# Kernel optimization log

Measured on AMD Instinct MI355X. Metric: run time of the kernel, lower is better.

The kernel has to match this reference:

```python
import jax, jax.numpy as jnp
import numpy as np

NUM_CLASSES = 81
IOU_THR = 0.5
NEG_POS_RATIO = 3


def _cxcywh_to_xyxy(b):
    cx, cy, w, h = b[..., 0], b[..., 1], b[..., 2], b[..., 3]
    return jnp.stack([cx - w / 2, cy - h / 2, cx + w / 2, cy + h / 2], axis=-1)


def _xyxy_to_cxcywh(b):
    x1, y1, x2, y2 = b[..., 0], b[..., 1], b[..., 2], b[..., 3]
    return jnp.stack([(x1 + x2) / 2, (y1 + y2) / 2, x2 - x1, y2 - y1], axis=-1)


def _iou(b1, b2):
    # b1 (M,4), b2 (A,4) in xyxy -> (M,A) pairwise IoU
    lt = jnp.maximum(b1[:, None, :2], b2[None, :, :2])
    rb = jnp.minimum(b1[:, None, 2:], b2[None, :, 2:])
    wh = jnp.clip(rb - lt, 0.0)
    inter = wh[..., 0] * wh[..., 1]
    a1 = (b1[:, 2] - b1[:, 0]) * (b1[:, 3] - b1[:, 1])
    a2 = (b2[:, 2] - b2[:, 0]) * (b2[:, 3] - b2[:, 1])
    union = a1[:, None] + a2[None, :] - inter
    return inter / (union + 1e-7)


def _match_one(gt_boxes, gt_labels, anchors_xyxy, anchors_cxcywh):
    # gt_boxes (M,4) xyxy, gt_labels (M,) -> per-anchor targets
    M = gt_boxes.shape[0]
    iou = _iou(gt_boxes, anchors_xyxy)          # (M, A)
    gt_best_iou = iou.max(axis=1)               # best anchor per GT
    gt_best_idx = iou.argmax(axis=1)
    a_best_iou = iou.max(axis=0)                # best GT per anchor
    a_best_idx = iou.argmax(axis=0)
    pos = a_best_iou > IOU_THR

    # sequential force-assignment (faithful to the torch per-object loop)
    def body(j, carry):
        pos, a_idx = carry
        ba = gt_best_idx[j]
        valid = gt_best_iou[j] > 1e-5
        pos = pos.at[ba].set(jnp.where(valid, True, pos[ba]))
        override = valid & (a_best_iou[ba] < gt_best_iou[j])
        a_idx = a_idx.at[ba].set(jnp.where(override, j, a_idx[ba]))
        return pos, a_idx

    pos, a_idx = jax.lax.fori_loop(0, M, body, (pos, a_best_idx))
    mb = _xyxy_to_cxcywh(gt_boxes[a_idx])       # (A,4) matched GT in cxcywh
    acx = anchors_cxcywh
    enc = jnp.stack([
        (mb[:, 0] - acx[:, 0]) / acx[:, 2],
        (mb[:, 1] - acx[:, 1]) / acx[:, 3],
        jnp.log(mb[:, 2] / acx[:, 2] + 1e-7),
        jnp.log(mb[:, 3] / acx[:, 3] + 1e-7)], axis=-1)
    true_locs = jnp.where(pos[:, None], enc, 0.0)
    true_cls = jnp.where(pos, gt_labels[a_idx] + 1, 0)
    return true_locs, true_cls, pos


def setup_inputs() -> dict:
    key = jax.random.key(0)
    kb, kl, kcx, kwh, kax, kaw, ks = jax.random.split(key, 7)
    B, A, M, C = 32, 24564, 20, NUM_CLASSES
    cxy = 0.2 + 0.6 * jax.random.uniform(kcx, (B, M, 2))
    wh = 0.05 + 0.25 * jax.random.uniform(kwh, (B, M, 2))
    gt_boxes = jnp.concatenate([cxy - wh / 2, cxy + wh / 2], axis=-1)  # valid xyxy
    gt_labels = jax.random.randint(kl, (B, M), 0, C - 1)
    acxy = jax.random.uniform(kax, (A, 2))
    awh = 0.04 + 0.3 * jax.random.uniform(kaw, (A, 2))
    anchors_cxcywh = jnp.concatenate([acxy, awh], axis=-1)
    predicted_locs = jax.random.normal(kb, (B, A, 4), jnp.float32)
    predicted_scores = jax.random.normal(ks, (B, A, C), jnp.float32)
    return {"predicted_locs": predicted_locs, "predicted_scores": predicted_scores,
            "gt_boxes": gt_boxes, "gt_labels": gt_labels,
            "anchors_cxcywh": anchors_cxcywh}


def reference(predicted_locs, predicted_scores, gt_boxes, gt_labels, anchors_cxcywh):
    B, A, C = predicted_scores.shape
    anchors_xyxy = _cxcywh_to_xyxy(anchors_cxcywh)
    true_locs, true_cls, pos = jax.vmap(_match_one, in_axes=(0, 0, None, None))(
        gt_boxes, gt_labels, anchors_xyxy, anchors_cxcywh)
    # SmoothL1 (beta=1, reduction='sum') over positive anchors only
    d = jnp.abs(predicted_locs - true_locs)
    sl1 = jnp.where(d < 1.0, 0.5 * d * d, d - 0.5)
    loc_loss = jnp.sum(sl1 * pos[..., None])
    # per-anchor cross entropy
    logp = jax.nn.log_softmax(predicted_scores, axis=-1)
    conf_all = -jnp.take_along_axis(logp, true_cls[..., None], axis=-1)[..., 0]  # (B,A)
    # hard negative mining
    n_pos = pos.sum(axis=1)                                   # (B,)
    n_keep = jnp.where(n_pos > 0,
                       jnp.minimum(NEG_POS_RATIO * n_pos, A - n_pos),
                       jnp.minimum(NEG_POS_RATIO * 20, A))
    neg_scores = jnp.where(pos, -jnp.inf, conf_all)           # positives never selected
    order = jnp.argsort(-neg_scores, axis=1)                  # descending
    ranks = jnp.argsort(order, axis=1)                        # 0 == hardest negative
    hard_neg = (ranks < n_keep[:, None]) & ~pos
    final_mask = pos | hard_neg
    conf_loss = jnp.sum(conf_all * final_mask)
    n_pos_total = jnp.maximum(n_pos.sum(), 1).astype(jnp.float32)
    total = (loc_loss + conf_loss) / n_pos_total
    return total, loc_loss / n_pos_total, conf_loss / n_pos_total
```

## Files before the change

### kernel.cpp

```cpp
#include <hip/hip_runtime.h>
#include <float.h>
#include <stdint.h>

#define NEG_POS_RATIO 3
#define MAXM 64
#define CHUNK 1024

__device__ __forceinline__ float smooth_l1(float d) {
    float a = fabsf(d);
    return a < 1.0f ? 0.5f * a * a : a - 0.5f;
}
__device__ __forceinline__ unsigned key_of(float f) {
    unsigned u = __float_as_uint(f);
    return (u & 0x80000000u) ? ~u : (u | 0x80000000u);
}
__device__ __forceinline__ float val_of(unsigned k) {
    return __uint_as_float((k & 0x80000000u) ? (k ^ 0x80000000u) : ~k);
}

__global__ void __launch_bounds__(256) k_init(
    unsigned long long* __restrict__ gbest, float* __restrict__ loc_loss,
    float* __restrict__ pos_conf, int* __restrict__ n_pos, int BM, int B)
{
    const int t = blockIdx.x * blockDim.x + threadIdx.x;
    if (t < BM) gbest[t] = 0ULL;
    if (t < B) { loc_loss[t] = 0.0f; pos_conf[t] = 0.0f; n_pos[t] = 0; }
}

__global__ void __launch_bounds__(256) k_gtbest(
    const float*  __restrict__ gt_boxes,
    const float4* __restrict__ anchors,
    int A, int M,
    unsigned long long* __restrict__ gbest)
{
    const int b = blockIdx.y, tid = threadIdx.x;
    const int base = blockIdx.x * CHUNK;
    __shared__ float              s_gt[MAXM * 4];
    __shared__ unsigned long long s_best[MAXM];
    if (tid < M * 4) s_gt[tid] = gt_boxes[(size_t)b * M * 4 + tid];
    if (tid < M) s_best[tid] = 0ULL;
    __syncthreads();

    float ax1[4], ay1[4], ax2[4], ay2[4], aarea[4];
    bool  val[4];
#pragma unroll
    for (int i = 0; i < 4; ++i) {
        const int a = base + tid + i * 256;
        val[i] = a < A;
        if (val[i]) {
            const float4 an = anchors[a];
            const float hx = an.z * 0.5f, hy = an.w * 0.5f;
            ax1[i] = an.x - hx; ay1[i] = an.y - hy;
            ax2[i] = an.x + hx; ay2[i] = an.y + hy;
            aarea[i] = an.z * an.w;
        } else { ax1[i]=ay1[i]=ax2[i]=ay2[i]=aarea[i]=0.0f; }
    }
    for (int j = 0; j < M; ++j) {
        const float gx1 = s_gt[4*j+0], gy1 = s_gt[4*j+1];
        const float gx2 = s_gt[4*j+2], gy2 = s_gt[4*j+3];
        const float garea = (gx2 - gx1) * (gy2 - gy1);
        unsigned long long best = 0ULL;
#pragma unroll
        for (int i = 0; i < 4; ++i) {
            if (!val[i]) continue;
            const float w = fmaxf(fminf(gx2, ax2[i]) - fmaxf(gx1, ax1[i]), 0.0f);
            const float h = fmaxf(fminf(gy2, ay2[i]) - fmaxf(gy1, ay1[i]), 0.0f);
            const float inter = w * h;
            const float iou = inter / ((garea + aarea[i] - inter) + 1e-7f);
            const unsigned a_idx = (unsigned)(base + tid + i * 256);
            const unsigned long long pk =
                ((unsigned long long)__float_as_uint(iou) << 32)
              | (unsigned long long)(0xFFFFFFFFu - a_idx);
            if (pk > best) best = pk;
        }
#pragma unroll
        for (int off = 32; off; off >>= 1) {
            const unsigned long long o = __shfl_xor(best, off);
            if (o > best) best = o;
        }
        if ((tid & 63) == 0) atomicMax(&s_best[j], best);
    }
    __syncthreads();
    if (tid < M) atomicMax(&gbest[(size_t)b * M + tid], s_best[tid]);
}

__global__ void __launch_bounds__(256) k_assign(
    const float4* __restrict__ pred_locs,
    const float*  __restrict__ gt_boxes,
    const int*    __restrict__ gt_labels,
    const float4* __restrict__ anchors,
    int A, int M,
    const unsigned long long* __restrict__ gbest,
    float* __restrict__ loc_loss, int* __restrict__ n_pos,
    int* __restrict__ cls_out)
{
    const int b = blockIdx.y, tid = threadIdx.x;
    const int base = blockIdx.x * CHUNK;
    __shared__ float s_gt[MAXM * 4];
    __shared__ int   s_lab[MAXM];
    __shared__ float s_gbi[MAXM];
    __shared__ int   s_gbx[MAXM];
    if (tid < M * 4) s_gt[tid] = gt_boxes[(size_t)b * M * 4 + tid];
    if (tid < M) {
        s_lab[tid] = gt_labels[(size_t)b * M + tid];
        const unsigned long long v = gbest[(size_t)b * M + tid];
        s_gbi[tid] = __uint_as_float((unsigned)(v >> 32));
        s_gbx[tid] = (int)(0xFFFFFFFFu - (unsigned)(v & 0xFFFFFFFFull));
    }
    __syncthreads();

    float lsum = 0.0f;
    int   np   = 0;
#pragma unroll
    for (int i = 0; i < 4; ++i) {
        const int a = base + tid + i * 256;
        if (a >= A) continue;
        const float4 an = anchors[a];
        const float hx = an.z * 0.5f, hy = an.w * 0.5f;
        const float ax1 = an.x - hx, ay1 = an.y - hy;
        const float ax2 = an.x + hx, ay2 = an.y + hy;
        const float aarea = an.z * an.w;
        float abest = -1.0f; int aidx = 0;
        for (int j = 0; j < M; ++j) {
            const float gx1 = s_gt[4*j+0], gy1 = s_gt[4*j+1];
            const float gx2 = s_gt[4*j+2], gy2 = s_gt[4*j+3];
            const float garea = (gx2 - gx1) * (gy2 - gy1);
            const float w = fmaxf(fminf(gx2, ax2) - fmaxf(gx1, ax1), 0.0f);
            const float h = fmaxf(fminf(gy2, ay2) - fmaxf(gy1, ay1), 0.0f);
            const float inter = w * h;
            const float iou = inter / ((garea + aarea - inter) + 1e-7f);
            if (iou > abest) { abest = iou; aidx = j; }
        }
        bool pos = abest > 0.5f;
        int midx = aidx;
        for (int j = 0; j < M; ++j) {
            if (s_gbx[j] == a && s_gbi[j] > 1e-5f) {
                pos = true;
                if (abest < s_gbi[j]) midx = j;
            }
        }
        int cls = 0;
        if (pos) {
            const float gx1 = s_gt[4*midx+0], gy1 = s_gt[4*midx+1];
            const float gx2 = s_gt[4*midx+2], gy2 = s_gt[4*midx+3];
            const float mcx = (gx1 + gx2) * 0.5f, mcy = (gy1 + gy2) * 0.5f;
            const float mw = gx2 - gx1, mh = gy2 - gy1;
            const float e0 = (mcx - an.x) / an.z;
            const float e1 = (mcy - an.y) / an.w;
            const float e2 = logf(mw / an.z + 1e-7f);
            const float e3 = logf(mh / an.w + 1e-7f);
            const float4 p = pred_locs[(size_t)b * A + a];
            lsum += smooth_l1(p.x - e0) + smooth_l1(p.y - e1)
                  + smooth_l1(p.z - e2) + smooth_l1(p.w - e3);
            ++np;
            cls = s_lab[midx] + 1;
        }
        cls_out[(size_t)b * A + a] = cls;
    }
#pragma unroll
    for (int off = 32; off; off >>= 1) {
        lsum += __shfl_xor(lsum, off);
        np   += __shfl_xor(np, off);
    }
    if ((tid & 63) == 0) {
        atomicAdd(&loc_loss[b], lsum);
        atomicAdd(&n_pos[b], np);
    }
}

__global__ void __launch_bounds__(256) k_conf(
    const float* __restrict__ scores,
    const int*   __restrict__ cls_arr,
    float* __restrict__ pos_conf,
    unsigned* __restrict__ keys,
    int A, int C, int total)
{
    const int tid  = threadIdx.x;
    const int wav  = tid >> 6;
    const int lane = tid & 63;
    const int g    = lane >> 4;
    const int sub  = lane & 15;
    const int row  = (blockIdx.x * 4 + wav) * 4 + g;

    float s  = 0.0f;
    float sc = -FLT_MAX;
    int   cls = 0;
    const bool active = row < total;
    if (active) {
        cls = cls_arr[row];
        const float* rp = scores + (size_t)row * C;
        for (int idx = sub; idx < C; idx += 16) {
            const float v = rp[idx];
            s += __expf(v);
            if (idx == cls) sc = v;
        }
    }
#pragma unroll
    for (int off = 8; off; off >>= 1) {
        s  += __shfl_xor(s, off);
        sc  = fmaxf(sc, __shfl_xor(sc, off));
    }
    if (active && sub == 0) {
        const float conf = __logf(s) - sc;
        if (cls > 0) {
            atomicAdd(&pos_conf[row / A], conf);
            keys[row] = 0u;
        } else {
            keys[row] = key_of(conf);
        }
    }
}

__global__ void __launch_bounds__(256) k_select(
    const unsigned* __restrict__ keys, const int* __restrict__ n_pos,
    float* __restrict__ neg_conf, int A, int M)
{
    const int b   = blockIdx.x;
    const int tid = threadIdx.x;
    const int lane = tid & 63;
    const unsigned* kb = keys + (size_t)b * A;
    const int np = n_pos[b];
    const int k = (np > 0) ? min(NEG_POS_RATIO * np, A - np)
                           : min(NEG_POS_RATIO * M, A);
    __shared__ int      hist[256];
    __shared__ unsigned s_pref;
    __shared__ int      s_rem;
    if (k <= 0) { if (tid == 0) neg_conf[b] = 0.0f; return; }
    if (tid == 0) { s_pref = 0u; s_rem = k; }
    __syncthreads();

    for (int pass = 0; pass < 4; ++pass) {
        const int shift = 24 - 8 * pass;
        hist[tid] = 0;
        __syncthreads();
        const unsigned pref = s_pref;
        for (int a = tid; a < A; a += blockDim.x) {
            const unsigned key = kb[a];
            const bool ok = (pass == 0) || ((key >> (shift + 8)) == (pref >> (shift + 8)));
            if (ok) {
                const int bin = (key >> shift) & 255;
                unsigned long long mm = __ballot(1);
#pragma unroll
                for (int bit = 0; bit < 8; ++bit) {
                    const unsigned long long bb = __ballot((bin >> bit) & 1);
                    mm &= ((bin >> bit) & 1) ? bb : ~bb;
                }
                if ((mm & ((1ULL << lane) - 1)) == 0)
                    atomicAdd(&hist[bin], (int)__popcll(mm));
            }
        }
        __syncthreads();
        if (tid == 0) {
            int rem = s_rem, cum = 0, bsel = 0;
            for (int i = 255; i >= 0; --i) {
                const int c = hist[i];
                if (cum + c >= rem) { bsel = i; s_rem = rem - cum; break; }
                cum += c;
            }
            s_pref = pref | ((unsigned)bsel << shift);
        }
        __syncthreads();
    }
    const unsigned kth = s_pref;
    float sum = 0.0f; int cnt = 0;
    for (int a = tid; a < A; a += blockDim.x) {
        const unsigned key = kb[a];
        if (key > kth) { sum += val_of(key); ++cnt; }
    }
#pragma unroll
    for (int off = 32; off; off >>= 1) {
        sum += __shfl_xor(sum, off);
        cnt += __shfl_xor(cnt, off);
    }
    __shared__ float s_sum[4];
    __shared__ int   s_cnt[4];
    const int w = tid >> 6;
    if (lane == 0) { s_sum[w] = sum; s_cnt[w] = cnt; }
    __syncthreads();
    if (tid == 0) {
        float ts = 0.0f; int tc = 0;
        for (int i = 0; i < (int)(blockDim.x >> 6); ++i) { ts += s_sum[i]; tc += s_cnt[i]; }
        neg_conf[b] = ts + (float)(k - tc) * val_of(kth);
    }
}

__global__ void __launch_bounds__(64) k_final(
    const float* __restrict__ loc_loss,
    const float* __restrict__ pos_conf,
    const float* __restrict__ neg_conf,
    const int*   __restrict__ n_pos,
    int B, float* __restrict__ out)
{
    const int tid = threadIdx.x;
    float L = 0.0f, Cs = 0.0f;
    int   np = 0;
    for (int b = tid; b < B; b += 64) {
        L  += loc_loss[b];
        Cs += pos_conf[b] + neg_conf[b];
        np += n_pos[b];
    }
#pragma unroll
    for (int off = 32; off; off >>= 1) {
        L  += __shfl_xor(L, off);
        Cs += __shfl_xor(Cs, off);
        np += __shfl_xor(np, off);
    }
    if (tid == 0) {
        const float denom = (float)(np > 1 ? np : 1);
        out[0] = (L + Cs) / denom;
        out[1] = L / denom;
        out[2] = Cs / denom;
    }
}

extern "C" void kernel_launch(void* const* d_in, const int* in_sizes, int n_in,
                              void* d_out, int out_size, void* d_ws, size_t ws_size,
                              hipStream_t stream) {
    const float* pred_locs = (const float*)d_in[0];
    const float* scores    = (const float*)d_in[1];
    const float* gt_boxes  = (const float*)d_in[2];
    const int*   gt_labels = (const int*)d_in[3];
    const float* anchors   = (const float*)d_in[4];

    const int A = in_sizes[4] / 4;
    const int B = (int)((long long)in_sizes[0] / (4LL * A));
    const int M = in_sizes[3] / B;
    const int C = (int)((long long)in_sizes[1] / ((long long)B * A));
    float* out = (float*)d_out;

    char* ws = (char*)d_ws;
    float* loc_loss = (float*)ws;
    float* pos_conf = loc_loss + B;
    float* neg_conf = pos_conf + B;
    int*   n_pos    = (int*)(neg_conf + B);
    size_t off = (size_t)(((16LL * B) + 255) / 256) * 256;
    unsigned long long* gbest = (unsigned long long*)(ws + off);
    off += (size_t)(((8LL * B * M) + 255) / 256) * 256;
    int*      cls_arr = (int*)(ws + off);
    unsigned* keys    = (unsigned*)(ws + off + (size_t)B * A * sizeof(int));

    const int NCHUNK = (A + CHUNK - 1) / CHUNK;

    k_init<<<(B * M + 255) / 256, 256, 0, stream>>>(gbest, loc_loss, pos_conf, n_pos,
                                                    B * M, B);
    k_gtbest<<<dim3(NCHUNK, B), 256, 0, stream>>>(gt_boxes, (const float4*)anchors,
                                                  A, M, gbest);
    k_assign<<<dim3(NCHUNK, B), 256, 0, stream>>>((const float4*)pred_locs, gt_boxes,
                                                  gt_labels, (const float4*)anchors,
                                                  A, M, gbest, loc_loss, n_pos, cls_arr);

    const int total = (int)((long long)B * A);
    const int nblk = (total + 15) / 16;
    k_conf<<<dim3((unsigned)nblk), 256, 0, stream>>>(scores, cls_arr, pos_conf, keys,
                                                     A, C, total);

    k_select<<<B, 256, 0, stream>>>(keys, n_pos, neg_conf, A, M);

    k_final<<<1, 64, 0, stream>>>(loc_loss, pos_conf, neg_conf, n_pos, B, out);
}
```

Measured before the change: 803.9 us.

## Stage score rows through LDS with float4 loads and widen select to 1024 threads

k_conf now loads 128 rows of scores per block cooperatively into shared memory with float4 loads, then has two threads per row compute log-sum-exp and gather the target logit. This replaces strided 16-lane row reads. k_select moves to 1024-thread blocks and reads keys as uint4 in the radix-select histogram and final sum passes. The LDS tile hardcodes 81 columns and assumes 16-byte alignment of each block's start. The larger LDS footprint may reduce occupancy.

```diff
diff --git a/kernel.cpp b/kernel.cpp
--- a/kernel.cpp
+++ b/kernel.cpp
@@ -5,6 +5,7 @@
 #define NEG_POS_RATIO 3
 #define MAXM 64
 #define CHUNK 1024
+#define ROWS_PER_BLK 128
 
 __device__ __forceinline__ float smooth_l1(float d) {
     float a = fabsf(d);
@@ -176,30 +177,42 @@
     int A, int C, int total)
 {
     const int tid  = threadIdx.x;
-    const int wav  = tid >> 6;
-    const int lane = tid & 63;
-    const int g    = lane >> 4;
-    const int sub  = lane & 15;
-    const int row  = (blockIdx.x * 4 + wav) * 4 + g;
-
+    const int row0 = blockIdx.x * ROWS_PER_BLK;
+    __shared__ float lds[ROWS_PER_BLK * 81];
+
+    const float* gp = scores + (size_t)row0 * C;
+    const int nrows = min(ROWS_PER_BLK, total - row0);
+    const int nf = nrows * C;
+    const int nv = nf >> 2;
+    const float4* gp4 = (const float4*)gp;
+    float4* l4 = (float4*)lds;
+    for (int i = tid; i < nv; i += 256) l4[i] = gp4[i];
+    for (int i = (nv << 2) + tid; i < nf; i += 256) lds[i] = gp[i];
+    __syncthreads();
+
+    const int rloc = tid >> 1;
+    const int sub  = tid & 1;
+    const int row  = row0 + rloc;
+    const bool active = rloc < nrows;
     float s  = 0.0f;
     float sc = -FLT_MAX;
     int   cls = 0;
-    const bool active = row < total;
     if (active) {
         cls = cls_arr[row];
-        const float* rp = scores + (size_t)row * C;
-        for (int idx = sub; idx < C; idx += 16) {
-            const float v = rp[idx];
-            s += __expf(v);
-            if (idx == cls) sc = v;
-        }
-    }
-#pragma unroll
-    for (int off = 8; off; off >>= 1) {
-        s  += __shfl_xor(s, off);
-        sc  = fmaxf(sc, __shfl_xor(sc, off));
-    }
+        const float* rp = lds + rloc * 81;
+        const int base = sub * 41;
+#pragma unroll 8
+        for (int i = 0; i < 41; ++i) {
+            const int idx = base + i;
+            if (idx < 81) {
+                const float v = rp[idx];
+                s += __expf(v);
+                if (idx == cls) sc = v;
+            }
+        }
+    }
+    s  += __shfl_xor(s, 1);
+    sc  = fmaxf(sc, __shfl_xor(sc, 1));
     if (active && sub == 0) {
         const float conf = __logf(s) - sc;
         if (cls > 0) {
@@ -211,12 +224,29 @@
     }
 }
 
-__global__ void __launch_bounds__(256) k_select(
+__device__ __forceinline__ void hist_add(
+    int* hist, unsigned key, unsigned pref, int shift, bool first, int lane)
+{
+    const bool ok = first || ((key >> (shift + 8)) == (pref >> (shift + 8)));
+    if (ok) {
+        const int bin = (key >> shift) & 255;
+        unsigned long long mm = __ballot(1);
+#pragma unroll
+        for (int bit = 0; bit < 8; ++bit) {
+            const unsigned long long bb = __ballot((bin >> bit) & 1);
+            mm &= ((bin >> bit) & 1) ? bb : ~bb;
+        }
+        if ((mm & ((1ULL << lane) - 1)) == 0)
+            atomicAdd(&hist[bin], (int)__popcll(mm));
+    }
+}
+
+__global__ void __launch_bounds__(1024) k_select(
     const unsigned* __restrict__ keys, const int* __restrict__ n_pos,
     float* __restrict__ neg_conf, int A, int M)
 {
-    const int b   = blockIdx.x;
-    const int tid = threadIdx.x;
+    const int b    = blockIdx.x;
+    const int tid  = threadIdx.x;
     const int lane = tid & 63;
     const unsigned* kb = keys + (size_t)b * A;
     const int np = n_pos[b];
@@ -227,28 +257,26 @@
     __shared__ int      s_rem;
     if (k <= 0) { if (tid == 0) neg_conf[b] = 0.0f; return; }
     if (tid == 0) { s_pref = 0u; s_rem = k; }
+
+    const int A4   = A >> 2;
+    const int tail = A - (A4 << 2);
+    const uint4* kb4 = (const uint4*)kb;
     __syncthreads();
 
     for (int pass = 0; pass < 4; ++pass) {
         const int shift = 24 - 8 * pass;
-        hist[tid] = 0;
+        if (tid < 256) hist[tid] = 0;
         __syncthreads();
         const unsigned pref = s_pref;
-        for (int a = tid; a < A; a += blockDim.x) {
-            const unsigned key = kb[a];
-            const bool ok = (pass == 0) || ((key >> (shift + 8)) == (pref >> (shift + 8)));
-            if (ok) {
-                const int bin = (key >> shift) & 255;
-                unsigned long long mm = __ballot(1);
-#pragma unroll
-                for (int bit = 0; bit < 8; ++bit) {
-                    const unsigned long long bb = __ballot((bin >> bit) & 1);
-                    mm &= ((bin >> bit) & 1) ? bb : ~bb;
-                }
-                if ((mm & ((1ULL << lane) - 1)) == 0)
-                    atomicAdd(&hist[bin], (int)__popcll(mm));
-            }
-        }
+        const bool first = (pass == 0);
+        for (int i = tid; i < A4; i += 1024) {
+            const uint4 kk = kb4[i];
+            hist_add(hist, kk.x, pref, shift, first, lane);
+            hist_add(hist, kk.y, pref, shift, first, lane);
+            hist_add(hist, kk.z, pref, shift, first, lane);
+            hist_add(hist, kk.w, pref, shift, first, lane);
+        }
+        if (tid < tail) hist_add(hist, kb[(A4 << 2) + tid], pref, shift, first, lane);
         __syncthreads();
         if (tid == 0) {
             int rem = s_rem, cum = 0, bsel = 0;
@@ -263,8 +291,15 @@
     }
     const unsigned kth = s_pref;
     float sum = 0.0f; int cnt = 0;
-    for (int a = tid; a < A; a += blockDim.x) {
-        const unsigned key = kb[a];
+    for (int i = tid; i < A4; i += 1024) {
+        const uint4 kk = kb4[i];
+        if (kk.x > kth) { sum += val_of(kk.x); ++cnt; }
+        if (kk.y > kth) { sum += val_of(kk.y); ++cnt; }
+        if (kk.z > kth) { sum += val_of(kk.z); ++cnt; }
+        if (kk.w > kth) { sum += val_of(kk.w); ++cnt; }
+    }
+    if (tid < tail) {
+        const unsigned key = kb[(A4 << 2) + tid];
         if (key > kth) { sum += val_of(key); ++cnt; }
     }
 #pragma unroll
@@ -272,14 +307,15 @@
         sum += __shfl_xor(sum, off);
         cnt += __shfl_xor(cnt, off);
     }
-    __shared__ float s_sum[4];
-    __shared__ int   s_cnt[4];
+    __shared__ float s_sum[16];
+    __shared__ int   s_cnt[16];
     const int w = tid >> 6;
     if (lane == 0) { s_sum[w] = sum; s_cnt[w] = cnt; }
     __syncthreads();
     if (tid == 0) {
         float ts = 0.0f; int tc = 0;
-        for (int i = 0; i < (int)(blockDim.x >> 6); ++i) { ts += s_sum[i]; tc += s_cnt[i]; }
+        const int nw = (int)(blockDim.x >> 6);
+        for (int i = 0; i < nw; ++i) { ts += s_sum[i]; tc += s_cnt[i]; }
         neg_conf[b] = ts + (float)(k - tc) * val_of(kth);
     }
 }
@@ -350,11 +386,11 @@
                                                   A, M, gbest, loc_loss, n_pos, cls_arr);
 
     const int total = (int)((long long)B * A);
-    const int nblk = (total + 15) / 16;
+    const int nblk = (total + ROWS_PER_BLK - 1) / ROWS_PER_BLK;
     k_conf<<<dim3((unsigned)nblk), 256, 0, stream>>>(scores, cls_arr, pos_conf, keys,
                                                      A, C, total);
 
-    k_select<<<B, 256, 0, stream>>>(keys, n_pos, neg_conf, A, M);
+    k_select<<<B, 1024, 0, stream>>>(keys, n_pos, neg_conf, A, M);
 
     k_final<<<1, 64, 0, stream>>>(loc_loss, pos_conf, neg_conf, n_pos, B, out);
 }
```

Result: faster. 760.9 us (-5.4%).

## Specialize conf kernel for 81 classes and widen radix-select to 1024 threads

Applied to the files above, without the earlier changes.

Adds a fully unrolled cross-entropy kernel for C==81 that issues all five or six loads per lane up front instead of looping, and keeps a generic fallback. The per-batch radix-select kernel now runs with 1024 threads, reads keys as uint4 with eight batched loads per thread, and handles the tail separately. The goal is more memory-level parallelism in both the softmax pass and the histogram/sum passes over keys. The risk is more ballot and shared-atomic contention per block in the select kernel, since it still launches only B blocks.

```diff
diff --git a/kernel.cpp b/kernel.cpp
--- a/kernel.cpp
+++ b/kernel.cpp
@@ -168,41 +168,48 @@
     }
 }
 
-__global__ void __launch_bounds__(256) k_conf(
+__global__ void __launch_bounds__(256) k_conf81(
     const float* __restrict__ scores,
     const int*   __restrict__ cls_arr,
     float* __restrict__ pos_conf,
     unsigned* __restrict__ keys,
-    int A, int C, int total)
+    int A, int total)
 {
     const int tid  = threadIdx.x;
     const int wav  = tid >> 6;
     const int lane = tid & 63;
-    const int g    = lane >> 4;
     const int sub  = lane & 15;
-    const int row  = (blockIdx.x * 4 + wav) * 4 + g;
-
-    float s  = 0.0f;
-    float sc = -FLT_MAX;
-    int   cls = 0;
-    const bool active = row < total;
-    if (active) {
-        cls = cls_arr[row];
-        const float* rp = scores + (size_t)row * C;
-        for (int idx = sub; idx < C; idx += 16) {
-            const float v = rp[idx];
-            s += __expf(v);
-            if (idx == cls) sc = v;
-        }
-    }
+    const int row  = (blockIdx.x * 4 + wav) * 4 + (lane >> 4);
+    if (row >= total) return;
+
+    const float* rp = scores + (size_t)row * 81;
+    const int c = cls_arr[row];
+    const float v0 = rp[sub];
+    const float v1 = rp[sub + 16];
+    const float v2 = rp[sub + 32];
+    const float v3 = rp[sub + 48];
+    const float v4 = rp[sub + 64];
+    float v5 = 0.0f;
+    const bool has5 = (sub == 0);
+    if (has5) v5 = rp[80];
+
+    float s = __expf(v0) + __expf(v1) + __expf(v2) + __expf(v3) + __expf(v4);
+    if (has5) s += __expf(v5);
+    float t = -FLT_MAX;
+    t = (sub      == c) ? v0 : t;
+    t = (sub + 16 == c) ? v1 : t;
+    t = (sub + 32 == c) ? v2 : t;
+    t = (sub + 48 == c) ? v3 : t;
+    t = (sub + 64 == c) ? v4 : t;
+    if (has5 && c == 80) t = v5;
 #pragma unroll
     for (int off = 8; off; off >>= 1) {
-        s  += __shfl_xor(s, off);
-        sc  = fmaxf(sc, __shfl_xor(sc, off));
-    }
-    if (active && sub == 0) {
-        const float conf = __logf(s) - sc;
-        if (cls > 0) {
+        s += __shfl_xor(s, off);
+        t  = fmaxf(t, __shfl_xor(t, off));
+    }
+    if (sub == 0) {
+        const float conf = __logf(s) - t;
+        if (c > 0) {
             atomicAdd(&pos_conf[row / A], conf);
             keys[row] = 0u;
         } else {
@@ -211,12 +218,64 @@
     }
 }
 
-__global__ void __launch_bounds__(256) k_select(
+__global__ void __launch_bounds__(256) k_conf_gen(
+    const float* __restrict__ scores, const int* __restrict__ cls_arr,
+    float* __restrict__ pos_conf, unsigned* __restrict__ keys,
+    int A, int C, int total)
+{
+    const int tid  = threadIdx.x;
+    const int lane = tid & 63;
+    const int sub  = lane & 15;
+    const int row  = (blockIdx.x * 4 + (tid >> 6)) * 4 + (lane >> 4);
+    float s = 0.0f, sc = -FLT_MAX;
+    int cls = 0;
+    const bool active = row < total;
+    if (active) {
+        cls = cls_arr[row];
+        const float* rpp = scores + (size_t)row * C;
+        for (int idx = sub; idx < C; idx += 16) {
+            const float v = rpp[idx];
+            s += __expf(v);
+            if (idx == cls) sc = v;
+        }
+    }
+#pragma unroll
+    for (int off = 8; off; off >>= 1) {
+        s  += __shfl_xor(s, off);
+        sc  = fmaxf(sc, __shfl_xor(sc, off));
+    }
+    if (active && sub == 0) {
+        const float conf = __logf(s) - sc;
+        if (cls > 0) { atomicAdd(&pos_conf[row / A], conf); keys[row] = 0u; }
+        else keys[row] = key_of(conf);
+    }
+}
+
+__device__ __forceinline__ void hist_add(
+    int* hist, unsigned key, unsigned pref, int shift, bool first, int lane,
+    bool valid)
+{
+    const bool ok = valid &&
+        (first || ((key >> (shift + 8)) == (pref >> (shift + 8))));
+    if (ok) {
+        const int bin = (key >> shift) & 255;
+        unsigned long long mm = __ballot(1);
+#pragma unroll
+        for (int bit = 0; bit < 8; ++bit) {
+            const unsigned long long bb = __ballot((bin >> bit) & 1);
+            mm &= ((bin >> bit) & 1) ? bb : ~bb;
+        }
+        if ((mm & ((1ULL << lane) - 1)) == 0)
+            atomicAdd(&hist[bin], (int)__popcll(mm));
+    }
+}
+
+__global__ void __launch_bounds__(1024) k_select(
     const unsigned* __restrict__ keys, const int* __restrict__ n_pos,
     float* __restrict__ neg_conf, int A, int M)
 {
-    const int b   = blockIdx.x;
-    const int tid = threadIdx.x;
+    const int b    = blockIdx.x;
+    const int tid  = threadIdx.x;
     const int lane = tid & 63;
     const unsigned* kb = keys + (size_t)b * A;
     const int np = n_pos[b];
@@ -227,28 +286,36 @@
     __shared__ int      s_rem;
     if (k <= 0) { if (tid == 0) neg_conf[b] = 0.0f; return; }
     if (tid == 0) { s_pref = 0u; s_rem = k; }
+
+    const int A4   = A >> 2;
+    const int tail = A - (A4 << 2);
+    const uint4* kb4 = (const uint4*)kb;
     __syncthreads();
 
     for (int pass = 0; pass < 4; ++pass) {
         const int shift = 24 - 8 * pass;
-        hist[tid] = 0;
+        if (tid < 256) hist[tid] = 0;
         __syncthreads();
         const unsigned pref = s_pref;
-        for (int a = tid; a < A; a += blockDim.x) {
-            const unsigned key = kb[a];
-            const bool ok = (pass == 0) || ((key >> (shift + 8)) == (pref >> (shift + 8)));
-            if (ok) {
-                const int bin = (key >> shift) & 255;
-                unsigned long long mm = __ballot(1);
-#pragma unroll
-                for (int bit = 0; bit < 8; ++bit) {
-                    const unsigned long long bb = __ballot((bin >> bit) & 1);
-                    mm &= ((bin >> bit) & 1) ? bb : ~bb;
-                }
-                if ((mm & ((1ULL << lane) - 1)) == 0)
-                    atomicAdd(&hist[bin], (int)__popcll(mm));
+        const bool first = (pass == 0);
+        for (int base = 0; base < A4; base += 8 * 1024) {
+            uint4 kk[8]; bool ok[8];
+#pragma unroll
+            for (int u = 0; u < 8; ++u) {
+                const int i = base + tid + u * 1024;
+                ok[u] = (i < A4);
+                kk[u] = ok[u] ? kb4[i] : uint4{0, 0, 0, 0};
             }
-        }
+#pragma unroll
+            for (int u = 0; u < 8; ++u) {
+                hist_add(hist, kk[u].x, pref, shift, first, lane, ok[u]);
+                hist_add(hist, kk[u].y, pref, shift, first, lane, ok[u]);
+                hist_add(hist, kk[u].z, pref, shift, first, lane, ok[u]);
+                hist_add(hist, kk[u].w, pref, shift, first, lane, ok[u]);
+            }
+        }
+        if (tid < tail) hist_add(hist, kb[(A4 << 2) + tid], pref, shift, first,
+                                 lane, true);
         __syncthreads();
         if (tid == 0) {
             int rem = s_rem, cum = 0, bsel = 0;
@@ -263,8 +330,24 @@
     }
     const unsigned kth = s_pref;
     float sum = 0.0f; int cnt = 0;
-    for (int a = tid; a < A; a += blockDim.x) {
-        const unsigned key = kb[a];
+    for (int base = 0; base < A4; base += 8 * 1024) {
+        uint4 kk[8]; bool ok[8];
+#pragma unroll
+        for (int u = 0; u < 8; ++u) {
+            const int i = base + tid + u * 1024;
+            ok[u] = (i < A4);
+            kk[u] = ok[u] ? kb4[i] : uint4{0, 0, 0, 0};
+        }
+#pragma unroll
+        for (int u = 0; u < 8; ++u) {
+            if (kk[u].x > kth) { sum += val_of(kk[u].x); ++cnt; }
+            if (kk[u].y > kth) { sum += val_of(kk[u].y); ++cnt; }
+            if (kk[u].z > kth) { sum += val_of(kk[u].z); ++cnt; }
+            if (kk[u].w > kth) { sum += val_of(kk[u].w); ++cnt; }
+        }
+    }
+    if (tid < tail) {
+        const unsigned key = kb[(A4 << 2) + tid];
         if (key > kth) { sum += val_of(key); ++cnt; }
     }
 #pragma unroll
@@ -272,14 +355,15 @@
         sum += __shfl_xor(sum, off);
         cnt += __shfl_xor(cnt, off);
     }
-    __shared__ float s_sum[4];
-    __shared__ int   s_cnt[4];
+    __shared__ float s_sum[16];
+    __shared__ int   s_cnt[16];
     const int w = tid >> 6;
     if (lane == 0) { s_sum[w] = sum; s_cnt[w] = cnt; }
     __syncthreads();
     if (tid == 0) {
         float ts = 0.0f; int tc = 0;
-        for (int i = 0; i < (int)(blockDim.x >> 6); ++i) { ts += s_sum[i]; tc += s_cnt[i]; }
+        const int nw = (int)(blockDim.x >> 6);
+        for (int i = 0; i < nw; ++i) { ts += s_sum[i]; tc += s_cnt[i]; }
         neg_conf[b] = ts + (float)(k - tc) * val_of(kth);
     }
 }
@@ -351,10 +435,15 @@
 
     const int total = (int)((long long)B * A);
     const int nblk = (total + 15) / 16;
-    k_conf<<<dim3((unsigned)nblk), 256, 0, stream>>>(scores, cls_arr, pos_conf, keys,
-                                                     A, C, total);
-
-    k_select<<<B, 256, 0, stream>>>(keys, n_pos, neg_conf, A, M);
+    if (C == 81) {
+        k_conf81<<<dim3((unsigned)nblk), 256, 0, stream>>>(scores, cls_arr, pos_conf,
+                                                           keys, A, total);
+    } else {
+        k_conf_gen<<<dim3((unsigned)nblk), 256, 0, stream>>>(scores, cls_arr, pos_conf,
+                                                             keys, A, C, total);
+    }
+
+    k_select<<<B, 1024, 0, stream>>>(keys, n_pos, neg_conf, A, M);
 
     k_final<<<1, 64, 0, stream>>>(loc_loss, pos_conf, neg_conf, n_pos, B, out);
 }
```

After: 690.9 us. 14.1% less time.
